# Optimization experiments

Measured on AMD Instinct MI355X. Metric: run time of the kernel, lower is better.

Reference implementation:

```python
import jax, jax.numpy as jnp
import numpy as np

# module hyper-parameters (VoronoiDecoder defaults)
S = 256          # n_seeds
Q = 262144       # query uv points
EPS = 1e-8
W_MIN = 0.005
BETA = 0.02
RAW_TEMP = 5.0
H_MIN, H_MAX = 0.5, 2.0
J_BETA_SCALE = 1.0
J_WIDTH_BONUS = 0.15
J_KEFF_K0 = 3.0
J_KEFF_S = 0.35
J_TRIPLE_LAMBDA = 0.15
J_TRIPLE_POWER = 1.5
KNN_K = 8
SOFTMIN_TAU = 0.002


def setup_inputs() -> dict:
    key = jax.random.key(0)
    ks = jax.random.split(key, 7)
    return {
        "uv": jax.random.uniform(ks[0], (Q, 2), jnp.float32),
        "seeds_raw": jax.random.uniform(ks[1], (S, 2), jnp.float32),
        "w_raw": jax.random.normal(ks[2], (S, S), jnp.float32),
        "h_raw": jax.random.normal(ks[3], (S,), jnp.float32),
        "theta": jax.random.normal(ks[4], (S,), jnp.float32),
        "a_raw": 0.3 * jax.random.normal(ks[5], (S,), jnp.float32),
        "seed_gates": jax.random.normal(ks[6], (S,), jnp.float32),
    }


def reference(uv, seeds_raw, w_raw, h_raw, theta, a_raw, seed_gates):
    seeds = seeds_raw  # seeds_uv is identity

    # --- pairwise seed distances (default buffers: all faces non-periodic,
    # seed_face_id all zero -> periodic wrap is a no-op -> plain euclidean) ---
    pd = jnp.linalg.norm(seeds[None, :, :] - seeds[:, None, :], axis=-1)  # (S,S)
    w_max_pair = jnp.maximum(0.8 * pd, W_MIN + EPS)
    w_geo = W_MIN + (w_max_pair - W_MIN) * jax.nn.sigmoid(w_raw / RAW_TEMP)
    W = 0.5 * (w_geo + w_geo.T)  # symmetric pairwise wall widths (S,S)

    h = H_MIN + (H_MAX - H_MIN) * jax.nn.sigmoid(h_raw)  # (S,) heights
    gates = jax.nn.sigmoid(seed_gates)                    # (S,) seed gates

    # --- anisotropic (unit-determinant) metric distance per seed ---
    c, sn = jnp.cos(theta), jnp.sin(theta)
    sc = jnp.exp(a_raw)  # anisotropy scale per seed
    dx = uv[:, None, 0] - seeds[None, :, 0]  # (Q,S)
    dy = uv[:, None, 1] - seeds[None, :, 1]
    xp = (c * dx + sn * dy) / sc   # rotate into seed frame, scale axes
    yp = (-sn * dx + c * dy) * sc
    d = jnp.sqrt(xp * xp + yp * yp + EPS)  # (Q,S) metric distances

    # --- kNN over seeds ---
    negk, idx = jax.lax.top_k(-d, KNN_K)   # (Q,K)
    dk = -negk
    d1, d3 = dk[:, 0], dk[:, 2]
    i1, i2 = idx[:, 0], idx[:, 1]
    w_pair = W[i1, i2]  # width of the wall between the 2 nearest cells

    # --- junction effects via softmin cell-membership weights ---
    p = jax.nn.softmax(-d / (BETA * J_BETA_SCALE), axis=-1)  # (Q,S)
    k_eff = 1.0 / (jnp.sum(p * p, axis=-1) + EPS)            # effective #cells
    bonus = J_WIDTH_BONUS * jax.nn.sigmoid((k_eff - J_KEFF_K0) / J_KEFF_S)
    triple = J_TRIPLE_LAMBDA * jnp.exp(-((d3 - d1) / (w_pair + EPS)) ** J_TRIPLE_POWER)
    w_eff = w_pair * (1.0 + bonus + triple)

    # --- softmin distance to Voronoi boundary over kNN bisectors ---
    b = 0.5 * (dk[:, 1:] - d1[:, None])  # (Q,K-1) bisector half-gaps
    sdist = -SOFTMIN_TAU * jax.nn.logsumexp(-b / SOFTMIN_TAU, axis=-1)
    wall = jax.nn.sigmoid((0.5 * w_eff - sdist) / BETA)  # shell occupancy

    h_blend = p @ h        # (Q,) blended height
    g_blend = p @ gates    # (Q,) blended gate
    return wall * g_blend * h_blend
```

## Files before the change

### kernel.cpp

```cpp
#include <hip/hip_runtime.h>

#define NSEED 256

typedef float v2f __attribute__((ext_vector_type(2)));
typedef float v4f __attribute__((ext_vector_type(4)));

__device__ __forceinline__ float fast_exp(float x) {
  return __builtin_amdgcn_exp2f(x * 1.4426950408889634f);
}
__device__ __forceinline__ float sigf(float x) {
  return 1.0f / (1.0f + fast_exp(-x));
}
__device__ __forceinline__ float med3(float x, float lo, float hi) {
  return __builtin_amdgcn_fmed3f(x, lo, hi);
}
__device__ __forceinline__ v2f vfma(v2f a, v2f b, v2f c) {
  return __builtin_elementwise_fma(a, b, c);
}

__global__ void seed_setup_kernel(const float* __restrict__ seeds,
                                  const float* __restrict__ h_raw,
                                  const float* __restrict__ theta,
                                  const float* __restrict__ a_raw,
                                  const float* __restrict__ seed_gates,
                                  float* __restrict__ Pg) {
  int s = threadIdx.x;
  if (s >= NSEED) return;
  float sx = seeds[2 * s], sy = seeds[2 * s + 1];
  float th = theta[s];
  float c = cosf(th), sn = sinf(th);
  float sc = expf(a_raw[s]);
  float inv = 1.0f / sc;
  float h = 0.5f + 1.5f * sigf(h_raw[s]);
  float g = sigf(seed_gates[s]);
  float* base = Pg + (s >> 1) * 16;
  int b = s & 1;
  base[0 + b] = sx;
  base[2 + b] = sy;
  base[4 + b] = c * inv;
  base[6 + b] = sn * inv;
  base[8 + b] = -sn * sc;
  base[10 + b] = c * sc;
  base[12 + b] = h;
  base[14 + b] = g;
}

__global__ __launch_bounds__(256) void voronoi_kernel(
    const float* __restrict__ uv, const float* __restrict__ seeds,
    const float* __restrict__ w_raw, const float* __restrict__ Pg,
    float* __restrict__ out, int nq) {
  const int q = blockIdx.x * 256 + threadIdx.x;
  if (q >= nq) return;
  const float2 uvq = ((const float2*)uv)[q];
  const v2f uu = {uvq.x, uvq.x}, vv = {uvq.y, uvq.y};
  const v2f eps2 = {1e-8f, 1e-8f};
  const float NK = -72.13475204444817f;

  float dk0 = 3e38f, dk1 = 3e38f, dk2 = 3e38f, dk3 = 3e38f;
  float dk4 = 3e38f, dk5 = 3e38f, dk6 = 3e38f, dk7 = 3e38f;
  int i0 = 0, i1 = 0;
  v2f S1 = {0.f, 0.f}, S2 = {0.f, 0.f}, Sh = {0.f, 0.f}, Sg = {0.f, 0.f};

#define INS(x, sidx)             \
  {                              \
    float _d = (x);              \
    bool c0 = _d < dk0;          \
    bool c1 = _d < dk1;          \
    int sh = c0 ? i0 : (sidx);   \
    i1 = c1 ? sh : i1;           \
    i0 = c0 ? (sidx) : i0;       \
    dk7 = med3(_d, dk6, dk7);    \
    dk6 = med3(_d, dk5, dk6);    \
    dk5 = med3(_d, dk4, dk5);    \
    dk4 = med3(_d, dk3, dk4);    \
    dk3 = med3(_d, dk2, dk3);    \
    dk2 = med3(_d, dk1, dk2);    \
    dk1 = med3(_d, dk0, dk1);    \
    dk0 = fminf(_d, dk0);        \
  }

  const v4f* __restrict__ PG = (const v4f*)Pg;
#pragma unroll 8
  for (int k = 0; k < NSEED / 2; ++k) {
    v4f q0 = PG[4 * k + 0];
    v4f q1 = PG[4 * k + 1];
    v4f q2 = PG[4 * k + 2];
    v4f q3 = PG[4 * k + 3];
    v2f dx = uu - q0.xy, dy = vv - q0.zw;
    v2f xp = vfma(q1.xy, dx, q1.zw * dy);
    v2f yp = vfma(q2.xy, dx, q2.zw * dy);
    v2f d2 = vfma(xp, xp, vfma(yp, yp, eps2));
    INS(d2.x, 2 * k);
    INS(d2.y, 2 * k + 1);
    float da = __builtin_amdgcn_sqrtf(d2.x);
    float db = __builtin_amdgcn_sqrtf(d2.y);
    v2f e;
    e.x = __builtin_amdgcn_exp2f(da * NK);
    e.y = __builtin_amdgcn_exp2f(db * NK);
    S1 += e;
    S2 = vfma(e, e, S2);
    Sh = vfma(e, q3.xy, Sh);
    Sg = vfma(e, q3.zw, Sg);
  }
#undef INS

  dk0 = __builtin_amdgcn_sqrtf(dk0);
  dk1 = __builtin_amdgcn_sqrtf(dk1);
  dk2 = __builtin_amdgcn_sqrtf(dk2);
  dk3 = __builtin_amdgcn_sqrtf(dk3);
  dk4 = __builtin_amdgcn_sqrtf(dk4);
  dk5 = __builtin_amdgcn_sqrtf(dk5);
  dk6 = __builtin_amdgcn_sqrtf(dk6);
  dk7 = __builtin_amdgcn_sqrtf(dk7);
  const float d1 = dk0, d3 = dk2;

  float S1s = S1.x + S1.y;
  float S2s = S2.x + S2.y;
  float Shs = Sh.x + Sh.y;
  float Sgs = Sg.x + Sg.y;

  float ax = seeds[2 * i0], ay = seeds[2 * i0 + 1];
  float bx = seeds[2 * i1], by = seeds[2 * i1 + 1];
  float pdx = ax - bx, pdy = ay - by;
  float pd = __builtin_amdgcn_sqrtf(fmaf(pdx, pdx, pdy * pdy));
  float wmax = fmaxf(0.8f * pd, 0.005f + 1e-8f);
  float wr01 = w_raw[(i0 << 8) + i1];
  float wr10 = w_raw[(i1 << 8) + i0];
  float w_pair = 0.005f + (wmax - 0.005f) * 0.5f * (sigf(wr01 * 0.2f) + sigf(wr10 * 0.2f));

  float s1sq = S1s * S1s;
  float keff = s1sq / fmaf(1e-8f, s1sq, S2s);
  float bonus = 0.15f * sigf((keff - 3.0f) * (1.0f / 0.35f));

  float tt = (d3 - d1) / (w_pair + 1e-8f);
  float t15 = tt * __builtin_amdgcn_sqrtf(tt);
  float triple = 0.15f * fast_exp(-t15);

  float w_eff = w_pair * (1.0f + bonus + triple);

  const float HT = 360.6737602222409f;
  float acc = 1.0f;
  acc += __builtin_amdgcn_exp2f((dk1 - dk2) * HT);
  acc += __builtin_amdgcn_exp2f((dk1 - dk3) * HT);
  acc += __builtin_amdgcn_exp2f((dk1 - dk4) * HT);
  acc += __builtin_amdgcn_exp2f((dk1 - dk5) * HT);
  acc += __builtin_amdgcn_exp2f((dk1 - dk6) * HT);
  acc += __builtin_amdgcn_exp2f((dk1 - dk7) * HT);
  float b1s = 0.5f * (dk1 - d1);
  float sdist = b1s - 0.002f * 0.6931471805599453f * __builtin_amdgcn_logf(acc);

  float wall = sigf((0.5f * w_eff - sdist) * 50.0f);
  float invS1 = 1.0f / S1s;
  out[q] = wall * (Sgs * invS1) * (Shs * invS1);
}

extern "C" void kernel_launch(void* const* d_in, const int* in_sizes, int n_in,
                              void* d_out, int out_size, void* d_ws, size_t ws_size,
                              hipStream_t stream) {
  (void)in_sizes;
  (void)n_in;
  (void)ws_size;
  const float* uv = (const float*)d_in[0];
  const float* seeds = (const float*)d_in[1];
  const float* w_raw = (const float*)d_in[2];
  const float* h_raw = (const float*)d_in[3];
  const float* theta = (const float*)d_in[4];
  const float* a_raw = (const float*)d_in[5];
  const float* gates = (const float*)d_in[6];
  float* out = (float*)d_out;
  float* Pg = (float*)d_ws;

  seed_setup_kernel<<<1, 256, 0, stream>>>(seeds, h_raw, theta, a_raw, gates, Pg);
  int nq = out_size;
  int grid = (nq + 255) / 256;
  voronoi_kernel<<<grid, 256, 0, stream>>>(uv, seeds, w_raw, Pg, out, nq);
}
```

Baseline: 114.6 us.

## Split seed loop across two waves per query and merge top-k via LDS

Each query is now processed by two wavefronts, each scanning half of the seeds, doubling the number of threads launched. The second wave writes its partial top-8 distances, nearest indices and softmax sums to shared memory, and the first wave merges them with a bitonic merge before the epilogue. This is meant to raise occupancy and latency hiding for the serial insertion chains. It adds an LDS exchange, a block barrier and half of the threads idling during the epilogue.

New measurement: 115.2 us. No clear change (+0.5%).

```diff
diff --git a/kernel.cpp b/kernel.cpp
--- a/kernel.cpp
+++ b/kernel.cpp
@@ -45,13 +45,20 @@
   base[14 + b] = g;
 }
 
-__global__ __launch_bounds__(256) void voronoi_kernel(
+__global__ __launch_bounds__(256, 8) void voronoi_kernel(
     const float* __restrict__ uv, const float* __restrict__ seeds,
     const float* __restrict__ w_raw, const float* __restrict__ Pg,
     float* __restrict__ out, int nq) {
-  const int q = blockIdx.x * 256 + threadIdx.x;
-  if (q >= nq) return;
-  const float2 uvq = ((const float2*)uv)[q];
+  __shared__ float LD[2][14][64];
+
+  const int wid = threadIdx.x >> 6;
+  const int lane = threadIdx.x & 63;
+  const int grp = wid >> 1;
+  const int half = wid & 1;
+  const int shalf = __builtin_amdgcn_readfirstlane(half);
+  const int q = blockIdx.x * 128 + grp * 64 + lane;
+  const int qc = q < nq ? q : nq - 1;
+  const float2 uvq = ((const float2*)uv)[qc];
   const v2f uu = {uvq.x, uvq.x}, vv = {uvq.y, uvq.y};
   const v2f eps2 = {1e-8f, 1e-8f};
   const float NK = -72.13475204444817f;
@@ -79,9 +86,9 @@
     dk0 = fminf(_d, dk0);        \
   }
 
-  const v4f* __restrict__ PG = (const v4f*)Pg;
+  const v4f* __restrict__ PG = (const v4f*)(Pg + shalf * 1024);
 #pragma unroll 8
-  for (int k = 0; k < NSEED / 2; ++k) {
+  for (int k = 0; k < 64; ++k) {
     v4f q0 = PG[4 * k + 0];
     v4f q1 = PG[4 * k + 1];
     v4f q2 = PG[4 * k + 2];
@@ -104,28 +111,85 @@
   }
 #undef INS
 
-  dk0 = __builtin_amdgcn_sqrtf(dk0);
-  dk1 = __builtin_amdgcn_sqrtf(dk1);
-  dk2 = __builtin_amdgcn_sqrtf(dk2);
-  dk3 = __builtin_amdgcn_sqrtf(dk3);
-  dk4 = __builtin_amdgcn_sqrtf(dk4);
-  dk5 = __builtin_amdgcn_sqrtf(dk5);
-  dk6 = __builtin_amdgcn_sqrtf(dk6);
-  dk7 = __builtin_amdgcn_sqrtf(dk7);
-  const float d1 = dk0, d3 = dk2;
+  i0 |= shalf << 7;
+  i1 |= shalf << 7;
 
   float S1s = S1.x + S1.y;
   float S2s = S2.x + S2.y;
   float Shs = Sh.x + Sh.y;
   float Sgs = Sg.x + Sg.y;
 
-  float ax = seeds[2 * i0], ay = seeds[2 * i0 + 1];
-  float bx = seeds[2 * i1], by = seeds[2 * i1 + 1];
+  if (half == 1) {
+    LD[grp][0][lane] = dk0;
+    LD[grp][1][lane] = dk1;
+    LD[grp][2][lane] = dk2;
+    LD[grp][3][lane] = dk3;
+    LD[grp][4][lane] = dk4;
+    LD[grp][5][lane] = dk5;
+    LD[grp][6][lane] = dk6;
+    LD[grp][7][lane] = dk7;
+    LD[grp][8][lane] = __int_as_float(i0);
+    LD[grp][9][lane] = __int_as_float(i1);
+    LD[grp][10][lane] = S1s;
+    LD[grp][11][lane] = S2s;
+    LD[grp][12][lane] = Shs;
+    LD[grp][13][lane] = Sgs;
+  }
+  __syncthreads();
+  if (half == 1 || q >= nq) return;
+
+  float b0 = LD[grp][0][lane], b1 = LD[grp][1][lane];
+  float b2 = LD[grp][2][lane], b3 = LD[grp][3][lane];
+  float b4 = LD[grp][4][lane], b5 = LD[grp][5][lane];
+  float b6 = LD[grp][6][lane], b7 = LD[grp][7][lane];
+  int j0 = __float_as_int(LD[grp][8][lane]);
+  int j1 = __float_as_int(LD[grp][9][lane]);
+  S1s += LD[grp][10][lane];
+  S2s += LD[grp][11][lane];
+  Shs += LD[grp][12][lane];
+  Sgs += LD[grp][13][lane];
+
+  bool aw = b0 < dk0;
+  float ec1 = aw ? dk0 : dk1;
+  int ic1 = aw ? i0 : i1;
+  float ec2 = aw ? b1 : b0;
+  int ic2 = aw ? j1 : j0;
+  const int I0 = aw ? j0 : i0;
+  const int I1 = (ec2 < ec1) ? ic2 : ic1;
+
+  float m0 = fminf(dk0, b7), m1 = fminf(dk1, b6);
+  float m2 = fminf(dk2, b5), m3 = fminf(dk3, b4);
+  float m4 = fminf(dk4, b3), m5 = fminf(dk5, b2);
+  float m6 = fminf(dk6, b1), m7 = fminf(dk7, b0);
+#define CE(a, b)             \
+  {                          \
+    float _lo = fminf(a, b); \
+    float _hi = fmaxf(a, b); \
+    a = _lo;                 \
+    b = _hi;                 \
+  }
+  CE(m0, m4) CE(m1, m5) CE(m2, m6) CE(m3, m7)
+  CE(m0, m2) CE(m1, m3) CE(m4, m6) CE(m5, m7)
+  CE(m0, m1) CE(m2, m3) CE(m4, m5) CE(m6, m7)
+#undef CE
+
+  dk0 = __builtin_amdgcn_sqrtf(m0);
+  dk1 = __builtin_amdgcn_sqrtf(m1);
+  dk2 = __builtin_amdgcn_sqrtf(m2);
+  dk3 = __builtin_amdgcn_sqrtf(m3);
+  dk4 = __builtin_amdgcn_sqrtf(m4);
+  dk5 = __builtin_amdgcn_sqrtf(m5);
+  dk6 = __builtin_amdgcn_sqrtf(m6);
+  dk7 = __builtin_amdgcn_sqrtf(m7);
+  const float d1 = dk0, d3 = dk2;
+
+  float ax = seeds[2 * I0], ay = seeds[2 * I0 + 1];
+  float bx = seeds[2 * I1], by = seeds[2 * I1 + 1];
   float pdx = ax - bx, pdy = ay - by;
   float pd = __builtin_amdgcn_sqrtf(fmaf(pdx, pdx, pdy * pdy));
   float wmax = fmaxf(0.8f * pd, 0.005f + 1e-8f);
-  float wr01 = w_raw[(i0 << 8) + i1];
-  float wr10 = w_raw[(i1 << 8) + i0];
+  float wr01 = w_raw[(I0 << 8) + I1];
+  float wr10 = w_raw[(I1 << 8) + I0];
   float w_pair = 0.005f + (wmax - 0.005f) * 0.5f * (sigf(wr01 * 0.2f) + sigf(wr10 * 0.2f));
 
   float s1sq = S1s * S1s;
@@ -172,6 +236,7 @@
 
   seed_setup_kernel<<<1, 256, 0, stream>>>(seeds, h_raw, theta, a_raw, gates, Pg);
   int nq = out_size;
-  int grid = (nq + 255) / 256;
+  long long threads = 2LL * nq;
+  int grid = (int)((threads + 255) / 256);
   voronoi_kernel<<<grid, 256, 0, stream>>>(uv, seeds, w_raw, Pg, out, nq);
 }
```

## Fold seed translation and softmax scale into transform, process two queries per thread

Applied to the files above, without the earlier changes.

The seed setup now precomputes an affine transform that includes the softmax temperature scale and the seed translation. The per-seed distance therefore drops the subtraction and the multiply before exp2, and the epilogue rescales the distances back. Each thread also handles two query points (t and t+nq/2) and shares the per-seed parameter loads between them, halving the grid. This costs more registers and may lower occupancy. If nq is odd, the last query would be dropped.

Result: slower. 127.2 us (+11.0%).

```diff
diff --git a/kernel.cpp b/kernel.cpp
--- a/kernel.cpp
+++ b/kernel.cpp
@@ -1,6 +1,8 @@
 #include <hip/hip_runtime.h>
 
 #define NSEED 256
+#define KBF 72.13475204444817f
+#define INV_KB 0.013862943611198906f
 
 typedef float v2f __attribute__((ext_vector_type(2)));
 typedef float v4f __attribute__((ext_vector_type(4)));
@@ -33,125 +35,139 @@
   float inv = 1.0f / sc;
   float h = 0.5f + 1.5f * sigf(h_raw[s]);
   float g = sigf(seed_gates[s]);
+  float A11 = KBF * c * inv, A12 = KBF * sn * inv;
+  float A21 = -KBF * sn * sc, A22 = KBF * c * sc;
+  float TX = -(A11 * sx + A12 * sy);
+  float TY = -(A21 * sx + A22 * sy);
   float* base = Pg + (s >> 1) * 16;
   int b = s & 1;
-  base[0 + b] = sx;
-  base[2 + b] = sy;
-  base[4 + b] = c * inv;
-  base[6 + b] = sn * inv;
-  base[8 + b] = -sn * sc;
-  base[10 + b] = c * sc;
+  base[0 + b] = A11;
+  base[2 + b] = A12;
+  base[4 + b] = A21;
+  base[6 + b] = A22;
+  base[8 + b] = TX;
+  base[10 + b] = TY;
   base[12 + b] = h;
   base[14 + b] = g;
 }
+
+#define INS(J, x, sidx)                      \
+  {                                          \
+    float _d = (x);                          \
+    bool c0 = _d < dk0##J;                   \
+    bool c1 = _d < dk1##J;                   \
+    int sh = c0 ? i0##J : (sidx);            \
+    i1##J = c1 ? sh : i1##J;                 \
+    i0##J = c0 ? (sidx) : i0##J;             \
+    dk7##J = med3(_d, dk6##J, dk7##J);       \
+    dk6##J = med3(_d, dk5##J, dk6##J);       \
+    dk5##J = med3(_d, dk4##J, dk5##J);       \
+    dk4##J = med3(_d, dk3##J, dk4##J);       \
+    dk3##J = med3(_d, dk2##J, dk3##J);       \
+    dk2##J = med3(_d, dk1##J, dk2##J);       \
+    dk1##J = med3(_d, dk0##J, dk1##J);       \
+    dk0##J = fminf(_d, dk0##J);              \
+  }
+
+#define PAIR_BODY(J, kk)                                        \
+  {                                                             \
+    v2f xp = vfma(q0.xy, uu##J, vfma(q2.xy, one2, q0.zw * vv##J)); \
+    v2f yp = vfma(q1.xy, uu##J, vfma(q2.zw, one2, q1.zw * vv##J)); \
+    v2f d2 = vfma(xp, xp, vfma(yp, yp, epsS));                  \
+    INS(J, d2.x, 2 * (kk))                                      \
+    INS(J, d2.y, 2 * (kk) + 1)                                  \
+    float da = __builtin_amdgcn_sqrtf(d2.x);                    \
+    float db = __builtin_amdgcn_sqrtf(d2.y);                    \
+    v2f e;                                                      \
+    e.x = __builtin_amdgcn_exp2f(-da);                          \
+    e.y = __builtin_amdgcn_exp2f(-db);                          \
+    S1##J += e;                                                 \
+    S2##J = vfma(e, e, S2##J);                                  \
+    Sh##J = vfma(e, q3.xy, Sh##J);                              \
+    Sg##J = vfma(e, q3.zw, Sg##J);                              \
+  }
+
+#define DECL_STATE(J)                                                      \
+  float dk0##J = 3e38f, dk1##J = 3e38f, dk2##J = 3e38f, dk3##J = 3e38f;    \
+  float dk4##J = 3e38f, dk5##J = 3e38f, dk6##J = 3e38f, dk7##J = 3e38f;    \
+  int i0##J = 0, i1##J = 0;                                                \
+  v2f S1##J = {0.f, 0.f}, S2##J = {0.f, 0.f};                              \
+  v2f Sh##J = {0.f, 0.f}, Sg##J = {0.f, 0.f};
+
+#define EPILOG(J, qidx)                                                        \
+  {                                                                            \
+    float e0 = __builtin_amdgcn_sqrtf(dk0##J);                                 \
+    float e1 = __builtin_amdgcn_sqrtf(dk1##J);                                 \
+    float e2 = __builtin_amdgcn_sqrtf(dk2##J);                                 \
+    float e3 = __builtin_amdgcn_sqrtf(dk3##J);                                 \
+    float e4 = __builtin_amdgcn_sqrtf(dk4##J);                                 \
+    float e5 = __builtin_amdgcn_sqrtf(dk5##J);                                 \
+    float e6 = __builtin_amdgcn_sqrtf(dk6##J);                                 \
+    float e7 = __builtin_amdgcn_sqrtf(dk7##J);                                 \
+    float S1s = S1##J.x + S1##J.y, S2s = S2##J.x + S2##J.y;                    \
+    float Shs = Sh##J.x + Sh##J.y, Sgs = Sg##J.x + Sg##J.y;                    \
+    int I0 = i0##J, I1 = i1##J;                                                \
+    float ax = seeds[2 * I0], ay = seeds[2 * I0 + 1];                          \
+    float bx = seeds[2 * I1], by = seeds[2 * I1 + 1];                          \
+    float pdx = ax - bx, pdy = ay - by;                                        \
+    float pd = __builtin_amdgcn_sqrtf(fmaf(pdx, pdx, pdy * pdy));              \
+    float wmax = fmaxf(0.8f * pd, 0.005f + 1e-8f);                             \
+    float wr01 = w_raw[(I0 << 8) + I1];                                        \
+    float wr10 = w_raw[(I1 << 8) + I0];                                        \
+    float w_pair =                                                             \
+        0.005f + (wmax - 0.005f) * 0.5f * (sigf(wr01 * 0.2f) + sigf(wr10 * 0.2f)); \
+    float s1sq = S1s * S1s;                                                    \
+    float keff = s1sq / fmaf(1e-8f, s1sq, S2s);                                \
+    float bonus = 0.15f * sigf((keff - 3.0f) * (1.0f / 0.35f));                \
+    float tt = (e2 - e0) * INV_KB / (w_pair + 1e-8f);                          \
+    float t15 = tt * __builtin_amdgcn_sqrtf(tt);                               \
+    float triple = 0.15f * fast_exp(-t15);                                     \
+    float w_eff = w_pair * (1.0f + bonus + triple);                            \
+    float acc = 1.0f;                                                          \
+    acc += __builtin_amdgcn_exp2f((e1 - e2) * 5.0f);                           \
+    acc += __builtin_amdgcn_exp2f((e1 - e3) * 5.0f);                           \
+    acc += __builtin_amdgcn_exp2f((e1 - e4) * 5.0f);                           \
+    acc += __builtin_amdgcn_exp2f((e1 - e5) * 5.0f);                           \
+    acc += __builtin_amdgcn_exp2f((e1 - e6) * 5.0f);                           \
+    acc += __builtin_amdgcn_exp2f((e1 - e7) * 5.0f);                           \
+    float b1s = (e1 - e0) * (0.5f * INV_KB);                                   \
+    float sdist = b1s - 0.002f * 0.6931471805599453f * __builtin_amdgcn_logf(acc); \
+    float wall = sigf((0.5f * w_eff - sdist) * 50.0f);                         \
+    float invS1 = 1.0f / S1s;                                                  \
+    out[qidx] = wall * (Sgs * invS1) * (Shs * invS1);                          \
+  }
 
 __global__ __launch_bounds__(256) void voronoi_kernel(
     const float* __restrict__ uv, const float* __restrict__ seeds,
     const float* __restrict__ w_raw, const float* __restrict__ Pg,
     float* __restrict__ out, int nq) {
-  const int q = blockIdx.x * 256 + threadIdx.x;
-  if (q >= nq) return;
-  const float2 uvq = ((const float2*)uv)[q];
-  const v2f uu = {uvq.x, uvq.x}, vv = {uvq.y, uvq.y};
-  const v2f eps2 = {1e-8f, 1e-8f};
-  const float NK = -72.13475204444817f;
+  const int halfq = nq >> 1;
+  const int t = blockIdx.x * 256 + threadIdx.x;
+  if (t >= halfq) return;
+  const int qA = t, qB = t + halfq;
+  const float2 uvA = ((const float2*)uv)[qA];
+  const float2 uvB = ((const float2*)uv)[qB];
+  const v2f uuA = {uvA.x, uvA.x}, vvA = {uvA.y, uvA.y};
+  const v2f uuB = {uvB.x, uvB.x}, vvB = {uvB.y, uvB.y};
+  const v2f epsS = {1e-8f * KBF * KBF, 1e-8f * KBF * KBF};
+  const v2f one2 = {1.0f, 1.0f};
 
-  float dk0 = 3e38f, dk1 = 3e38f, dk2 = 3e38f, dk3 = 3e38f;
-  float dk4 = 3e38f, dk5 = 3e38f, dk6 = 3e38f, dk7 = 3e38f;
-  int i0 = 0, i1 = 0;
-  v2f S1 = {0.f, 0.f}, S2 = {0.f, 0.f}, Sh = {0.f, 0.f}, Sg = {0.f, 0.f};
-
-#define INS(x, sidx)             \
-  {                              \
-    float _d = (x);              \
-    bool c0 = _d < dk0;          \
-    bool c1 = _d < dk1;          \
-    int sh = c0 ? i0 : (sidx);   \
-    i1 = c1 ? sh : i1;           \
-    i0 = c0 ? (sidx) : i0;       \
-    dk7 = med3(_d, dk6, dk7);    \
-    dk6 = med3(_d, dk5, dk6);    \
-    dk5 = med3(_d, dk4, dk5);    \
-    dk4 = med3(_d, dk3, dk4);    \
-    dk3 = med3(_d, dk2, dk3);    \
-    dk2 = med3(_d, dk1, dk2);    \
-    dk1 = med3(_d, dk0, dk1);    \
-    dk0 = fminf(_d, dk0);        \
-  }
+  DECL_STATE(A)
+  DECL_STATE(B)
 
   const v4f* __restrict__ PG = (const v4f*)Pg;
-#pragma unroll 8
+#pragma unroll 4
   for (int k = 0; k < NSEED / 2; ++k) {
     v4f q0 = PG[4 * k + 0];
     v4f q1 = PG[4 * k + 1];
     v4f q2 = PG[4 * k + 2];
     v4f q3 = PG[4 * k + 3];
-    v2f dx = uu - q0.xy, dy = vv - q0.zw;
-    v2f xp = vfma(q1.xy, dx, q1.zw * dy);
-    v2f yp = vfma(q2.xy, dx, q2.zw * dy);
-    v2f d2 = vfma(xp, xp, vfma(yp, yp, eps2));
-    INS(d2.x, 2 * k);
-    INS(d2.y, 2 * k + 1);
-    float da = __builtin_amdgcn_sqrtf(d2.x);
-    float db = __builtin_amdgcn_sqrtf(d2.y);
-    v2f e;
-    e.x = __builtin_amdgcn_exp2f(da * NK);
-    e.y = __builtin_amdgcn_exp2f(db * NK);
-    S1 += e;
-    S2 = vfma(e, e, S2);
-    Sh = vfma(e, q3.xy, Sh);
-    Sg = vfma(e, q3.zw, Sg);
+    PAIR_BODY(A, k)
+    PAIR_BODY(B, k)
   }
-#undef INS
 
-  dk0 = __builtin_amdgcn_sqrtf(dk0);
-  dk1 = __builtin_amdgcn_sqrtf(dk1);
-  dk2 = __builtin_amdgcn_sqrtf(dk2);
-  dk3 = __builtin_amdgcn_sqrtf(dk3);
-  dk4 = __builtin_amdgcn_sqrtf(dk4);
-  dk5 = __builtin_amdgcn_sqrtf(dk5);
-  dk6 = __builtin_amdgcn_sqrtf(dk6);
-  dk7 = __builtin_amdgcn_sqrtf(dk7);
-  const float d1 = dk0, d3 = dk2;
-
-  float S1s = S1.x + S1.y;
-  float S2s = S2.x + S2.y;
-  float Shs = Sh.x + Sh.y;
-  float Sgs = Sg.x + Sg.y;
-
-  float ax = seeds[2 * i0], ay = seeds[2 * i0 + 1];
-  float bx = seeds[2 * i1], by = seeds[2 * i1 + 1];
-  float pdx = ax - bx, pdy = ay - by;
-  float pd = __builtin_amdgcn_sqrtf(fmaf(pdx, pdx, pdy * pdy));
-  float wmax = fmaxf(0.8f * pd, 0.005f + 1e-8f);
-  float wr01 = w_raw[(i0 << 8) + i1];
-  float wr10 = w_raw[(i1 << 8) + i0];
-  float w_pair = 0.005f + (wmax - 0.005f) * 0.5f * (sigf(wr01 * 0.2f) + sigf(wr10 * 0.2f));
-
-  float s1sq = S1s * S1s;
-  float keff = s1sq / fmaf(1e-8f, s1sq, S2s);
-  float bonus = 0.15f * sigf((keff - 3.0f) * (1.0f / 0.35f));
-
-  float tt = (d3 - d1) / (w_pair + 1e-8f);
-  float t15 = tt * __builtin_amdgcn_sqrtf(tt);
-  float triple = 0.15f * fast_exp(-t15);
-
-  float w_eff = w_pair * (1.0f + bonus + triple);
-
-  const float HT = 360.6737602222409f;
-  float acc = 1.0f;
-  acc += __builtin_amdgcn_exp2f((dk1 - dk2) * HT);
-  acc += __builtin_amdgcn_exp2f((dk1 - dk3) * HT);
-  acc += __builtin_amdgcn_exp2f((dk1 - dk4) * HT);
-  acc += __builtin_amdgcn_exp2f((dk1 - dk5) * HT);
-  acc += __builtin_amdgcn_exp2f((dk1 - dk6) * HT);
-  acc += __builtin_amdgcn_exp2f((dk1 - dk7) * HT);
-  float b1s = 0.5f * (dk1 - d1);
-  float sdist = b1s - 0.002f * 0.6931471805599453f * __builtin_amdgcn_logf(acc);
-
-  float wall = sigf((0.5f * w_eff - sdist) * 50.0f);
-  float invS1 = 1.0f / S1s;
-  out[q] = wall * (Sgs * invS1) * (Shs * invS1);
+  EPILOG(A, qA)
+  EPILOG(B, qB)
 }
 
 extern "C" void kernel_launch(void* const* d_in, const int* in_sizes, int n_in,
@@ -172,6 +188,7 @@
 
   seed_setup_kernel<<<1, 256, 0, stream>>>(seeds, h_raw, theta, a_raw, gates, Pg);
   int nq = out_size;
-  int grid = (nq + 255) / 256;
+  int halfq = nq >> 1;
+  int grid = (halfq + 255) / 256;
   voronoi_kernel<<<grid, 256, 0, stream>>>(uv, seeds, w_raw, Pg, out, nq);
 }
```
